# Optimization experiments

Hardware: AMD Instinct MI355X
Metric: run time of the kernel (lower is better)

## Reference

```python
import jax, jax.numpy as jnp
import numpy as np

N, E, IN, HID, H, L, CLS = 10000, 160000, 512, 128, 8, 4, 2
ALPHA = 0.1  # residual weight
BN_EPS = 1e-5
NEG_SLOPE = 0.2  # PyG GATConv leaky_relu default


def setup_inputs() -> dict:
    key = jax.random.key(0)
    ks = jax.random.split(key, 16)
    s = 0.05
    return {
        "x": jax.random.normal(ks[0], (N, IN), jnp.float32),
        "edge_index": jax.random.randint(ks[1], (2, E), 0, N, jnp.int64),
        "Wp": jax.random.normal(ks[2], (IN, HID), jnp.float32) * s,
        "bp": jax.random.normal(ks[3], (HID,), jnp.float32) * s,
        # stacked per-layer GATConv params (shared src/dst weight as in PyG)
        "Wl": jax.random.normal(ks[4], (L, HID, H * HID), jnp.float32) * s,
        "att_src": jax.random.normal(ks[5], (L, H, HID), jnp.float32) * s,
        "att_dst": jax.random.normal(ks[6], (L, H, HID), jnp.float32) * s,
        "bl": jax.random.normal(ks[7], (L, HID), jnp.float32) * s,
        # BatchNorm (eval mode: running_mean=0, running_var=1)
        "gamma": 1.0 + jax.random.normal(ks[8], (L, HID), jnp.float32) * s,
        "beta": jax.random.normal(ks[9], (L, HID), jnp.float32) * s,
        # classifier
        "W1": jax.random.normal(ks[10], (HID, HID // 2), jnp.float32) * s,
        "b1": jax.random.normal(ks[11], (HID // 2,), jnp.float32) * s,
        "W2": jax.random.normal(ks[12], (HID // 2, CLS), jnp.float32) * s,
        "b2": jax.random.normal(ks[13], (CLS,), jnp.float32) * s,
    }


def gat_layer(h, src, dst, W, a_src, a_dst, bias):
    # h: [N, HID]; W: [HID, H*HID]
    xl = (h @ W).reshape(N, H, HID)                 # [N, H, C]
    alpha_s = jnp.sum(xl * a_src[None], axis=-1)     # [N, H]
    alpha_d = jnp.sum(xl * a_dst[None], axis=-1)     # [N, H]
    e = jax.nn.leaky_relu(alpha_s[src] + alpha_d[dst], NEG_SLOPE)  # [E', H]
    # segment softmax over incoming edges of each dst node
    emax = jax.ops.segment_max(e, dst, num_segments=N)
    ee = jnp.exp(e - emax[dst])
    denom = jax.ops.segment_sum(ee, dst, num_segments=N)
    att = ee / (denom[dst] + 1e-16)                  # [E', H]
    msg = xl[src] * att[:, :, None]                  # [E', H, C]
    out = jax.ops.segment_sum(msg, dst, num_segments=N)  # [N, H, C]
    return out.mean(axis=1) + bias                   # concat=False -> mean over heads


def reference(x, edge_index, Wp, bp, Wl, att_src, att_dst, bl, gamma, beta, W1, b1, W2, b2):
    # add self-loops (PyG GATConv default add_self_loops=True)
    loop = jnp.arange(N, dtype=edge_index.dtype)
    src = jnp.concatenate([edge_index[0], loop])
    dst = jnp.concatenate([edge_index[1], loop])

    h = jax.nn.elu(x @ Wp + bp)
    bn_inv = 1.0 / jnp.sqrt(1.0 + BN_EPS)
    for i in range(L):
        prev = h
        g = gat_layer(h, src, dst, Wl[i], att_src[i], att_dst[i], bl[i])
        g = gamma[i] * (g * bn_inv) + beta[i]        # BN eval (mean 0, var 1)
        h = jax.nn.elu((1.0 - ALPHA) * g + ALPHA * prev)
        # dropout is identity in eval mode
    hid = jax.nn.elu(h @ W1 + b1)
    return hid @ W2 + b2                             # [N, CLS]
```

## Files before the change

kernel.cpp:

```cpp
#include <hip/hip_runtime.h>
#include <cstdint>
#include <cstddef>

#define N_NODES 10000
#define N_EDGES 160000
#define DIM_IN  512
#define HIDDIM  128
#define NHEAD   8
#define NLAYER  4

typedef unsigned int  uint32;
typedef unsigned short ushort16;

static __device__ __forceinline__ float eluf(float v)  { return v > 0.f ? v : expm1f(v); }
static __device__ __forceinline__ float lrelu(float v) { return v >= 0.f ? v : 0.2f * v; }
static __device__ __forceinline__ ushort16 f2bf(float f) {
    uint32 u = __float_as_uint(f);
    u += 0x7fffu + ((u >> 16) & 1u);
    return (ushort16)(u >> 16);
}

#define BN_INV 0.9999950000374997f

__global__ void k_deg(const int* __restrict__ ei, int* __restrict__ deg) {
    int t = blockIdx.x * 256 + threadIdx.x;
    if (t < N_EDGES) atomicAdd(&deg[ei[N_EDGES + t]], 1);
}

__global__ __launch_bounds__(1024) void k_scan(const int* __restrict__ deg,
                                               int* __restrict__ rowptr,
                                               int* __restrict__ cursor) {
    __shared__ int sd[1024];
    __shared__ int carry;
    int tid = threadIdx.x;
    if (tid == 0) { carry = 0; rowptr[0] = 0; }
    __syncthreads();
    for (int base = 0; base < N_NODES; base += 1024) {
        int i = base + tid;
        int v = (i < N_NODES) ? (deg[i] + 1) : 0;
        sd[tid] = v;
        __syncthreads();
        for (int ofs = 1; ofs < 1024; ofs <<= 1) {
            int t = (tid >= ofs) ? sd[tid - ofs] : 0;
            __syncthreads();
            sd[tid] += t;
            __syncthreads();
        }
        int inc = sd[tid] + carry;
        if (i < N_NODES) { rowptr[i + 1] = inc; cursor[i] = inc - v; }
        __syncthreads();
        if (tid == 1023) carry = inc;
        __syncthreads();
    }
}

__global__ void k_scatter(const int* __restrict__ ei, int* __restrict__ cursor,
                          int* __restrict__ csr) {
    int t = blockIdx.x * 256 + threadIdx.x;
    if (t < N_EDGES) {
        int s = ei[t];
        int d = ei[N_EDGES + t];
        int p = atomicAdd(&cursor[d], 1);
        csr[p] = s;
    } else if (t < N_EDGES + N_NODES) {
        int n = t - N_EDGES;
        int p = atomicAdd(&cursor[n], 1);
        csr[p] = n;
    }
}

template <int ACT, int OUTBF>
__global__ __launch_bounds__(256) void k_gemm(const float* __restrict__ A,
                                              const float* __restrict__ B,
                                              const float* __restrict__ bias,
                                              void* __restrict__ Cv,
                                              int M, int Nn, int K) {
    __shared__ float As[16][64];
    __shared__ float Bs[16][64];
    const int tx = threadIdx.x & 15;
    const int ty = threadIdx.x >> 4;
    const int row0 = blockIdx.y * 64, col0 = blockIdx.x * 64;
    const int la_m = threadIdx.x >> 2;
    const int la_k = (threadIdx.x & 3) * 4;
    const int lb_k = threadIdx.x >> 4;
    const int lb_n = (threadIdx.x & 15) * 4;
    float acc[4][4] = {};
    for (int k0 = 0; k0 < K; k0 += 16) {
        float4 av = make_float4(0.f, 0.f, 0.f, 0.f);
        int ar = row0 + la_m;
        if (ar < M) av = *(const float4*)(A + (size_t)ar * K + k0 + la_k);
        As[la_k + 0][la_m] = av.x;
        As[la_k + 1][la_m] = av.y;
        As[la_k + 2][la_m] = av.z;
        As[la_k + 3][la_m] = av.w;
        *(float4*)&Bs[lb_k][lb_n] = *(const float4*)(B + (size_t)(k0 + lb_k) * Nn + col0 + lb_n);
        __syncthreads();
#pragma unroll
        for (int k = 0; k < 16; k++) {
            float a[4], b[4];
#pragma unroll
            for (int i = 0; i < 4; i++) a[i] = As[k][ty * 4 + i];
#pragma unroll
            for (int j = 0; j < 4; j++) b[j] = Bs[k][tx * 4 + j];
#pragma unroll
            for (int i = 0; i < 4; i++)
#pragma unroll
                for (int j = 0; j < 4; j++) acc[i][j] += a[i] * b[j];
        }
        __syncthreads();
    }
#pragma unroll
    for (int i = 0; i < 4; i++) {
        int r = row0 + ty * 4 + i;
        if (r < M) {
            if (OUTBF) {
                ushort4 o;
                o.x = f2bf(acc[i][0]);
                o.y = f2bf(acc[i][1]);
                o.z = f2bf(acc[i][2]);
                o.w = f2bf(acc[i][3]);
                *(ushort4*)((ushort16*)Cv + (size_t)r * Nn + col0 + tx * 4) = o;
            } else {
                float4 o;
                float* op = (float*)&o;
#pragma unroll
                for (int j = 0; j < 4; j++) {
                    float v = acc[i][j];
                    if (ACT) {
                        v += bias[col0 + tx * 4 + j];
                        v = eluf(v);
                    }
                    op[j] = v;
                }
                *(float4*)((float*)Cv + (size_t)r * Nn + col0 + tx * 4) = o;
            }
        }
    }
}

__global__ __launch_bounds__(256) void k_alphas(const ushort16* __restrict__ xl,
                                                const float* __restrict__ atts,
                                                const float* __restrict__ attd,
                                                float* __restrict__ as_,
                                                float* __restrict__ ad_) {
    int lane = threadIdx.x & 63;
    int n = blockIdx.x * 4 + (threadIdx.x >> 6);
    if (n >= N_NODES) return;
    int g = lane >> 4;
    int c8 = 8 * (lane & 15);
    const uint4* xp = (const uint4*)(xl + (size_t)n * 1024);
    float ss[2], sd[2];
#pragma unroll
    for (int j = 0; j < 2; j++) {
        int head = 4 * j + g;
        uint4 u = xp[j * 64 + lane];
        const float4* ap = (const float4*)(atts + head * 128 + c8);
        const float4* bp = (const float4*)(attd + head * 128 + c8);
        float4 a0 = ap[0], a1 = ap[1];
        float4 b0 = bp[0], b1 = bp[1];
        float x0 = __uint_as_float(u.x << 16), x1 = __uint_as_float(u.x & 0xffff0000u);
        float x2 = __uint_as_float(u.y << 16), x3 = __uint_as_float(u.y & 0xffff0000u);
        float x4 = __uint_as_float(u.z << 16), x5 = __uint_as_float(u.z & 0xffff0000u);
        float x6 = __uint_as_float(u.w << 16), x7 = __uint_as_float(u.w & 0xffff0000u);
        ss[j] = x0 * a0.x + x1 * a0.y + x2 * a0.z + x3 * a0.w +
                x4 * a1.x + x5 * a1.y + x6 * a1.z + x7 * a1.w;
        sd[j] = x0 * b0.x + x1 * b0.y + x2 * b0.z + x3 * b0.w +
                x4 * b1.x + x5 * b1.y + x6 * b1.z + x7 * b1.w;
    }
#pragma unroll
    for (int m = 1; m < 16; m <<= 1) {
#pragma unroll
        for (int j = 0; j < 2; j++) {
            ss[j] += __shfl_xor(ss[j], m);
            sd[j] += __shfl_xor(sd[j], m);
        }
    }
    if ((lane & 15) == 0) {
        as_[n * 8 + g]     = ss[0];
        as_[n * 8 + 4 + g] = ss[1];
        ad_[n * 8 + g]     = sd[0];
        ad_[n * 8 + 4 + g] = sd[1];
    }
}

__global__ __launch_bounds__(256) void k_aggregate(const int* __restrict__ rowptr,
                                                   const int* __restrict__ csr,
                                                   const float* __restrict__ as_,
                                                   const float* __restrict__ ad_,
                                                   const ushort16* __restrict__ xl,
                                                   const float* __restrict__ hprev,
                                                   const float* __restrict__ bl,
                                                   const float* __restrict__ gam,
                                                   const float* __restrict__ bet,
                                                   float* __restrict__ hnext) {
    int lane = threadIdx.x & 63;
    int n = blockIdx.x * 4 + (threadIdx.x >> 6);
    if (n >= N_NODES) return;
    int h8 = lane & 7;
    int g = lane >> 4;
    float adh = ad_[n * 8 + h8];
    int start = rowptr[n], end = rowptr[n + 1];

    float acc0[8] = {}, acc1[8] = {};
    float denom = 0.f;
    int s = (start < end) ? csr[start] : 0;
    for (int e = start; e < end; ++e) {
        int sn = (e + 1 < end) ? csr[e + 1] : 0;
        float t = lrelu(as_[s * 8 + h8] + adh);
        float ee = __expf(t);
        denom += ee;
        float e0 = __shfl(ee, g);
        float e1 = __shfl(ee, 4 + g);
        const uint4* xp = (const uint4*)(xl + (size_t)s * 1024);
        uint4 u0 = xp[lane];
        uint4 u1 = xp[64 + lane];
        acc0[0] += e0 * __uint_as_float(u0.x << 16);
        acc0[1] += e0 * __uint_as_float(u0.x & 0xffff0000u);
        acc0[2] += e0 * __uint_as_float(u0.y << 16);
        acc0[3] += e0 * __uint_as_float(u0.y & 0xffff0000u);
        acc0[4] += e0 * __uint_as_float(u0.z << 16);
        acc0[5] += e0 * __uint_as_float(u0.z & 0xffff0000u);
        acc0[6] += e0 * __uint_as_float(u0.w << 16);
        acc0[7] += e0 * __uint_as_float(u0.w & 0xffff0000u);
        acc1[0] += e1 * __uint_as_float(u1.x << 16);
        acc1[1] += e1 * __uint_as_float(u1.x & 0xffff0000u);
        acc1[2] += e1 * __uint_as_float(u1.y << 16);
        acc1[3] += e1 * __uint_as_float(u1.y & 0xffff0000u);
        acc1[4] += e1 * __uint_as_float(u1.z << 16);
        acc1[5] += e1 * __uint_as_float(u1.z & 0xffff0000u);
        acc1[6] += e1 * __uint_as_float(u1.w << 16);
        acc1[7] += e1 * __uint_as_float(u1.w & 0xffff0000u);
        s = sn;
    }

    float d0 = __shfl(denom, g);
    float d1 = __shfl(denom, 4 + g);
    float r0 = 1.f / (d0 + 1e-16f);
    float r1 = 1.f / (d1 + 1e-16f);
    float sum[8];
#pragma unroll
    for (int i = 0; i < 8; i++) sum[i] = acc0[i] * r0 + acc1[i] * r1;
#pragma unroll
    for (int i = 0; i < 8; i++) {
        sum[i] += __shfl_xor(sum[i], 16);
        sum[i] += __shfl_xor(sum[i], 32);
    }

    if (lane < 16) {
        int c = 8 * lane;
        float o[8];
#pragma unroll
        for (int t = 0; t < 8; t++) {
            float m = sum[t] * 0.125f + bl[c + t];
            float gg = gam[c + t] * (m * BN_INV) + bet[c + t];
            float z = 0.9f * gg + 0.1f * hprev[(size_t)n * 128 + c + t];
            o[t] = eluf(z);
        }
        *(float4*)(hnext + (size_t)n * 128 + c)     = make_float4(o[0], o[1], o[2], o[3]);
        *(float4*)(hnext + (size_t)n * 128 + c + 4) = make_float4(o[4], o[5], o[6], o[7]);
    }
}

__global__ __launch_bounds__(256) void k_classifier(const float* __restrict__ h,
                                                    const float* __restrict__ W1,
                                                    const float* __restrict__ b1,
                                                    const float* __restrict__ W2,
                                                    const float* __restrict__ b2,
                                                    float* __restrict__ out) {
    __shared__ float sW1[128 * 64];
    __shared__ float sW2[128];
    __shared__ float sb1[64];
    __shared__ float sb2[2];
    for (int i = threadIdx.x; i < 2048; i += 256)
        *(float4*)&sW1[i * 4] = *(const float4*)(W1 + i * 4);
    if (threadIdx.x < 64) sb1[threadIdx.x] = b1[threadIdx.x];
    if (threadIdx.x < 128) sW2[threadIdx.x] = W2[threadIdx.x];
    if (threadIdx.x < 2) sb2[threadIdx.x] = b2[threadIdx.x];
    __syncthreads();
    int lane = threadIdx.x & 63;
    int n = blockIdx.x * 4 + (threadIdx.x >> 6);
    if (n >= N_NODES) return;
    float h0 = h[(size_t)n * 128 + lane];
    float h1 = h[(size_t)n * 128 + 64 + lane];
    float acc = sb1[lane];
#pragma unroll
    for (int c = 0; c < 64; c++) acc += __shfl(h0, c) * sW1[c * 64 + lane];
#pragma unroll
    for (int c = 0; c < 64; c++) acc += __shfl(h1, c) * sW1[(64 + c) * 64 + lane];
    acc = eluf(acc);
    float p0 = acc * sW2[lane * 2 + 0];
    float p1 = acc * sW2[lane * 2 + 1];
#pragma unroll
    for (int m = 1; m < 64; m <<= 1) {
        p0 += __shfl_xor(p0, m);
        p1 += __shfl_xor(p1, m);
    }
    if (lane == 0) {
        out[(size_t)n * 2 + 0] = p0 + sb2[0];
        out[(size_t)n * 2 + 1] = p1 + sb2[1];
    }
}

extern "C" void kernel_launch(void* const* d_in, const int* in_sizes, int n_in,
                              void* d_out, int out_size, void* d_ws, size_t ws_size,
                              hipStream_t stream) {
    const float* x       = (const float*)d_in[0];
    const int* ei        = (const int*)d_in[1];
    const float* Wp      = (const float*)d_in[2];
    const float* bp      = (const float*)d_in[3];
    const float* Wl      = (const float*)d_in[4];
    const float* atts    = (const float*)d_in[5];
    const float* attd    = (const float*)d_in[6];
    const float* bl      = (const float*)d_in[7];
    const float* gam     = (const float*)d_in[8];
    const float* bet     = (const float*)d_in[9];
    const float* W1      = (const float*)d_in[10];
    const float* b1      = (const float*)d_in[11];
    const float* W2      = (const float*)d_in[12];
    const float* b2      = (const float*)d_in[13];
    float* out = (float*)d_out;

    char* w = (char*)d_ws;
    auto carve = [&](size_t bytes) -> void* {
        void* p = (void*)w;
        w += (bytes + 255) & ~(size_t)255;
        return p;
    };
    int* deg        = (int*)carve((size_t)N_NODES * 4);
    int* rowptr     = (int*)carve((size_t)(N_NODES + 1) * 4);
    int* cursor     = (int*)carve((size_t)N_NODES * 4);
    int* csr        = (int*)carve((size_t)(N_EDGES + N_NODES) * 4);
    float* as_      = (float*)carve((size_t)N_NODES * 8 * 4);
    float* ad_      = (float*)carve((size_t)N_NODES * 8 * 4);
    ushort16* xl    = (ushort16*)carve((size_t)N_NODES * 1024 * 2);
    float* hA       = (float*)carve((size_t)N_NODES * 128 * 4);
    float* hB       = (float*)carve((size_t)N_NODES * 128 * 4);

    hipMemsetAsync(deg, 0, (size_t)N_NODES * 4, stream);
    k_deg<<<(N_EDGES + 255) / 256, 256, 0, stream>>>(ei, deg);
    k_scan<<<1, 1024, 0, stream>>>(deg, rowptr, cursor);
    k_scatter<<<(N_EDGES + N_NODES + 255) / 256, 256, 0, stream>>>(ei, cursor, csr);

    k_gemm<1, 0><<<dim3(2, 157), 256, 0, stream>>>(x, Wp, bp, hA, N_NODES, 128, 512);

    float* hc = hA;
    float* hn = hB;
    for (int l = 0; l < NLAYER; l++) {
        k_gemm<0, 1><<<dim3(16, 157), 256, 0, stream>>>(hc, Wl + (size_t)l * 128 * 1024, nullptr,
                                                        xl, N_NODES, 1024, 128);
        k_alphas<<<2500, 256, 0, stream>>>(xl, atts + l * 1024, attd + l * 1024, as_, ad_);
        k_aggregate<<<2500, 256, 0, stream>>>(rowptr, csr, as_, ad_, xl, hc, bl + l * 128,
                                              gam + l * 128, bet + l * 128, hn);
        float* tmp = hc; hc = hn; hn = tmp;
    }
    k_classifier<<<2500, 256, 0, stream>>>(hc, W1, b1, W2, b2, out);
}
```

Measured before the change: 585.1 us.

## Use bf16 MFMA GEMM with swizzled LDS and unroll aggregation loop by two

Replaces the scalar FP32 tiled GEMM with a bf16 MFMA 16x16x32 kernel. It stages A and B tiles in LDS as bf16 with an XOR swizzle and a K-tile of 128, so the projection and per-layer GATConv matmuls run on matrix cores. The aggregate loop is also unrolled two edges at a time so gathers for two neighbours are in flight together. Rounding inputs to bf16 lowers GEMM precision, including the first projection, which was FP32 before.

```diff
diff --git a/kernel.cpp b/kernel.cpp
--- a/kernel.cpp
+++ b/kernel.cpp
@@ -9,8 +9,10 @@
 #define NHEAD   8
 #define NLAYER  4
 
-typedef unsigned int  uint32;
+typedef unsigned int   uint32;
 typedef unsigned short ushort16;
+typedef __attribute__((ext_vector_type(8))) short bf16x8;
+typedef __attribute__((ext_vector_type(4))) float f32x4;
 
 static __device__ __forceinline__ float eluf(float v)  { return v > 0.f ? v : expm1f(v); }
 static __device__ __forceinline__ float lrelu(float v) { return v >= 0.f ? v : 0.2f * v; }
@@ -19,6 +21,8 @@
     u += 0x7fffu + ((u >> 16) & 1u);
     return (ushort16)(u >> 16);
 }
+static __device__ __forceinline__ float blo(uint32 u) { return __uint_as_float(u << 16); }
+static __device__ __forceinline__ float bhi(uint32 u) { return __uint_as_float(u & 0xffff0000u); }
 
 #define BN_INV 0.9999950000374997f
 
@@ -70,69 +74,79 @@
 }
 
 template <int ACT, int OUTBF>
-__global__ __launch_bounds__(256) void k_gemm(const float* __restrict__ A,
-                                              const float* __restrict__ B,
-                                              const float* __restrict__ bias,
-                                              void* __restrict__ Cv,
-                                              int M, int Nn, int K) {
-    __shared__ float As[16][64];
-    __shared__ float Bs[16][64];
-    const int tx = threadIdx.x & 15;
-    const int ty = threadIdx.x >> 4;
+__global__ __launch_bounds__(256) void k_gemm_mfma(const float* __restrict__ A,
+                                                   const float* __restrict__ B,
+                                                   const float* __restrict__ bias,
+                                                   void* __restrict__ Cv,
+                                                   int M, int Nn, int K) {
+    __shared__ unsigned short AsU[64 * 128];
+    __shared__ unsigned short BsU[64 * 128];
+    char* AsB = (char*)AsU;
+    char* BsB = (char*)BsU;
+    const int tid = threadIdx.x;
+    const int lane = tid & 63;
+    const int wv = tid >> 6;
     const int row0 = blockIdx.y * 64, col0 = blockIdx.x * 64;
-    const int la_m = threadIdx.x >> 2;
-    const int la_k = (threadIdx.x & 3) * 4;
-    const int lb_k = threadIdx.x >> 4;
-    const int lb_n = (threadIdx.x & 15) * 4;
-    float acc[4][4] = {};
-    for (int k0 = 0; k0 < K; k0 += 16) {
-        float4 av = make_float4(0.f, 0.f, 0.f, 0.f);
-        int ar = row0 + la_m;
-        if (ar < M) av = *(const float4*)(A + (size_t)ar * K + k0 + la_k);
-        As[la_k + 0][la_m] = av.x;
-        As[la_k + 1][la_m] = av.y;
-        As[la_k + 2][la_m] = av.z;
-        As[la_k + 3][la_m] = av.w;
-        *(float4*)&Bs[lb_k][lb_n] = *(const float4*)(B + (size_t)(k0 + lb_k) * Nn + col0 + lb_n);
-        __syncthreads();
-#pragma unroll
-        for (int k = 0; k < 16; k++) {
-            float a[4], b[4];
-#pragma unroll
-            for (int i = 0; i < 4; i++) a[i] = As[k][ty * 4 + i];
-#pragma unroll
-            for (int j = 0; j < 4; j++) b[j] = Bs[k][tx * 4 + j];
-#pragma unroll
-            for (int i = 0; i < 4; i++)
-#pragma unroll
-                for (int j = 0; j < 4; j++) acc[i][j] += a[i] * b[j];
-        }
-        __syncthreads();
-    }
-#pragma unroll
-    for (int i = 0; i < 4; i++) {
-        int r = row0 + ty * 4 + i;
-        if (r < M) {
-            if (OUTBF) {
-                ushort4 o;
-                o.x = f2bf(acc[i][0]);
-                o.y = f2bf(acc[i][1]);
-                o.z = f2bf(acc[i][2]);
-                o.w = f2bf(acc[i][3]);
-                *(ushort4*)((ushort16*)Cv + (size_t)r * Nn + col0 + tx * 4) = o;
-            } else {
-                float4 o;
-                float* op = (float*)&o;
-#pragma unroll
-                for (int j = 0; j < 4; j++) {
-                    float v = acc[i][j];
-                    if (ACT) {
-                        v += bias[col0 + tx * 4 + j];
-                        v = eluf(v);
-                    }
-                    op[j] = v;
-                }
-                *(float4*)((float*)Cv + (size_t)r * Nn + col0 + tx * 4) = o;
+    const int r = lane & 15, q = lane >> 4;
+
+    f32x4 acc[4];
+#pragma unroll
+    for (int i = 0; i < 4; i++) acc[i] = (f32x4){0.f, 0.f, 0.f, 0.f};
+
+    for (int k0 = 0; k0 < K; k0 += 128) {
+        __syncthreads();
+#pragma unroll
+        for (int it = 0; it < 8; it++) {
+            int gq = tid + it * 256;
+            int row = gq >> 5;
+            int k4 = (gq & 31) * 4;
+            int gr = row0 + row;
+            float4 v = make_float4(0.f, 0.f, 0.f, 0.f);
+            if (gr < M) v = *(const float4*)(A + (size_t)gr * K + k0 + k4);
+            ushort4 o;
+            o.x = f2bf(v.x); o.y = f2bf(v.y); o.z = f2bf(v.z); o.w = f2bf(v.w);
+            int byte = (row * 256 + k4 * 2) ^ ((row & 7) << 4);
+            *(ushort4*)(AsB + byte) = o;
+        }
+#pragma unroll
+        for (int it = 0; it < 8; it++) {
+            int gq = tid + it * 256;
+            int kk = gq >> 4;
+            int c4 = (gq & 15) * 4;
+            float4 v = *(const float4*)(B + (size_t)(k0 + kk) * Nn + col0 + c4);
+            float vv[4] = {v.x, v.y, v.z, v.w};
+#pragma unroll
+            for (int c = 0; c < 4; c++) {
+                int col = c4 + c;
+                int byte = (col * 256 + kk * 2) ^ ((col & 7) << 4);
+                *(unsigned short*)(BsB + byte) = f2bf(vv[c]);
+            }
+        }
+        __syncthreads();
+#pragma unroll
+        for (int ks = 0; ks < 4; ks++) {
+            int kb = (ks * 32 + q * 8) * 2;
+            int arow = wv * 16 + r;
+            bf16x8 af = *(bf16x8*)(AsB + ((arow * 256 + kb) ^ ((arow & 7) << 4)));
+#pragma unroll
+            for (int nb = 0; nb < 4; nb++) {
+                int col = nb * 16 + r;
+                bf16x8 bfr = *(bf16x8*)(BsB + ((col * 256 + kb) ^ ((col & 7) << 4)));
+                acc[nb] = __builtin_amdgcn_mfma_f32_16x16x32_bf16(af, bfr, acc[nb], 0, 0, 0);
+            }
+        }
+    }
+#pragma unroll
+    for (int nb = 0; nb < 4; nb++) {
+        int col = col0 + nb * 16 + r;
+#pragma unroll
+        for (int j = 0; j < 4; j++) {
+            int row = row0 + wv * 16 + q * 4 + j;
+            if (row < M) {
+                float v = acc[nb][j];
+                if (ACT) { v += bias[col]; v = eluf(v); }
+                if (OUTBF) ((unsigned short*)Cv)[(size_t)row * Nn + col] = f2bf(v);
+                else       ((float*)Cv)[(size_t)row * Nn + col] = v;
             }
         }
     }
@@ -158,10 +172,8 @@
         const float4* bp = (const float4*)(attd + head * 128 + c8);
         float4 a0 = ap[0], a1 = ap[1];
         float4 b0 = bp[0], b1 = bp[1];
-        float x0 = __uint_as_float(u.x << 16), x1 = __uint_as_float(u.x & 0xffff0000u);
-        float x2 = __uint_as_float(u.y << 16), x3 = __uint_as_float(u.y & 0xffff0000u);
-        float x4 = __uint_as_float(u.z << 16), x5 = __uint_as_float(u.z & 0xffff0000u);
-        float x6 = __uint_as_float(u.w << 16), x7 = __uint_as_float(u.w & 0xffff0000u);
+        float x0 = blo(u.x), x1 = bhi(u.x), x2 = blo(u.y), x3 = bhi(u.y);
+        float x4 = blo(u.z), x5 = bhi(u.z), x6 = blo(u.w), x7 = bhi(u.w);
         ss[j] = x0 * a0.x + x1 * a0.y + x2 * a0.z + x3 * a0.w +
                 x4 * a1.x + x5 * a1.y + x6 * a1.z + x7 * a1.w;
         sd[j] = x0 * b0.x + x1 * b0.y + x2 * b0.z + x3 * b0.w +
@@ -203,34 +215,56 @@
 
     float acc0[8] = {}, acc1[8] = {};
     float denom = 0.f;
-    int s = (start < end) ? csr[start] : 0;
-    for (int e = start; e < end; ++e) {
-        int sn = (e + 1 < end) ? csr[e + 1] : 0;
-        float t = lrelu(as_[s * 8 + h8] + adh);
-        float ee = __expf(t);
-        denom += ee;
-        float e0 = __shfl(ee, g);
-        float e1 = __shfl(ee, 4 + g);
-        const uint4* xp = (const uint4*)(xl + (size_t)s * 1024);
-        uint4 u0 = xp[lane];
-        uint4 u1 = xp[64 + lane];
-        acc0[0] += e0 * __uint_as_float(u0.x << 16);
-        acc0[1] += e0 * __uint_as_float(u0.x & 0xffff0000u);
-        acc0[2] += e0 * __uint_as_float(u0.y << 16);
-        acc0[3] += e0 * __uint_as_float(u0.y & 0xffff0000u);
-        acc0[4] += e0 * __uint_as_float(u0.z << 16);
-        acc0[5] += e0 * __uint_as_float(u0.z & 0xffff0000u);
-        acc0[6] += e0 * __uint_as_float(u0.w << 16);
-        acc0[7] += e0 * __uint_as_float(u0.w & 0xffff0000u);
-        acc1[0] += e1 * __uint_as_float(u1.x << 16);
-        acc1[1] += e1 * __uint_as_float(u1.x & 0xffff0000u);
-        acc1[2] += e1 * __uint_as_float(u1.y << 16);
-        acc1[3] += e1 * __uint_as_float(u1.y & 0xffff0000u);
-        acc1[4] += e1 * __uint_as_float(u1.z << 16);
-        acc1[5] += e1 * __uint_as_float(u1.z & 0xffff0000u);
-        acc1[6] += e1 * __uint_as_float(u1.w << 16);
-        acc1[7] += e1 * __uint_as_float(u1.w & 0xffff0000u);
-        s = sn;
+    int e = start;
+    int s0 = csr[e];
+    int s1 = (e + 1 < end) ? csr[e + 1] : 0;
+    for (; e + 1 < end; e += 2) {
+        int s2 = (e + 2 < end) ? csr[e + 2] : 0;
+        int s3 = (e + 3 < end) ? csr[e + 3] : 0;
+        float as0 = as_[s0 * 8 + h8];
+        float as1 = as_[s1 * 8 + h8];
+        const uint4* xp0 = (const uint4*)(xl + (size_t)s0 * 1024);
+        const uint4* xp1 = (const uint4*)(xl + (size_t)s1 * 1024);
+        uint4 u0a = xp0[lane], u1a = xp0[64 + lane];
+        uint4 u0b = xp1[lane], u1b = xp1[64 + lane];
+        float ee0 = __expf(lrelu(as0 + adh));
+        float ee1 = __expf(lrelu(as1 + adh));
+        denom += ee0 + ee1;
+        float e0a = __shfl(ee0, g), e1a = __shfl(ee0, 4 + g);
+        float e0b = __shfl(ee1, g), e1b = __shfl(ee1, 4 + g);
+        acc0[0] += e0a * blo(u0a.x); acc0[1] += e0a * bhi(u0a.x);
+        acc0[2] += e0a * blo(u0a.y); acc0[3] += e0a * bhi(u0a.y);
+        acc0[4] += e0a * blo(u0a.z); acc0[5] += e0a * bhi(u0a.z);
+        acc0[6] += e0a * blo(u0a.w); acc0[7] += e0a * bhi(u0a.w);
+        acc1[0] += e1a * blo(u1a.x); acc1[1] += e1a * bhi(u1a.x);
+        acc1[2] += e1a * blo(u1a.y); acc1[3] += e1a * bhi(u1a.y);
+        acc1[4] += e1a * blo(u1a.z); acc1[5] += e1a * bhi(u1a.z);
+        acc1[6] += e1a * blo(u1a.w); acc1[7] += e1a * bhi(u1a.w);
+        acc0[0] += e0b * blo(u0b.x); acc0[1] += e0b * bhi(u0b.x);
+        acc0[2] += e0b * blo(u0b.y); acc0[3] += e0b * bhi(u0b.y);
+        acc0[4] += e0b * blo(u0b.z); acc0[5] += e0b * bhi(u0b.z);
+        acc0[6] += e0b * blo(u0b.w); acc0[7] += e0b * bhi(u0b.w);
+        acc1[0] += e1b * blo(u1b.x); acc1[1] += e1b * bhi(u1b.x);
+        acc1[2] += e1b * blo(u1b.y); acc1[3] += e1b * bhi(u1b.y);
+        acc1[4] += e1b * blo(u1b.z); acc1[5] += e1b * bhi(u1b.z);
+        acc1[6] += e1b * blo(u1b.w); acc1[7] += e1b * bhi(u1b.w);
+        s0 = s2; s1 = s3;
+    }
+    if (e < end) {
+        float as0 = as_[s0 * 8 + h8];
+        const uint4* xp0 = (const uint4*)(xl + (size_t)s0 * 1024);
+        uint4 u0a = xp0[lane], u1a = xp0[64 + lane];
+        float ee0 = __expf(lrelu(as0 + adh));
+        denom += ee0;
+        float e0a = __shfl(ee0, g), e1a = __shfl(ee0, 4 + g);
+        acc0[0] += e0a * blo(u0a.x); acc0[1] += e0a * bhi(u0a.x);
+        acc0[2] += e0a * blo(u0a.y); acc0[3] += e0a * bhi(u0a.y);
+        acc0[4] += e0a * blo(u0a.z); acc0[5] += e0a * bhi(u0a.z);
+        acc0[6] += e0a * blo(u0a.w); acc0[7] += e0a * bhi(u0a.w);
+        acc1[0] += e1a * blo(u1a.x); acc1[1] += e1a * bhi(u1a.x);
+        acc1[2] += e1a * blo(u1a.y); acc1[3] += e1a * bhi(u1a.y);
+        acc1[4] += e1a * blo(u1a.z); acc1[5] += e1a * bhi(u1a.z);
+        acc1[6] += e1a * blo(u1a.w); acc1[7] += e1a * bhi(u1a.w);
     }
 
     float d0 = __shfl(denom, g);
@@ -341,13 +375,13 @@
     k_scan<<<1, 1024, 0, stream>>>(deg, rowptr, cursor);
     k_scatter<<<(N_EDGES + N_NODES + 255) / 256, 256, 0, stream>>>(ei, cursor, csr);
 
-    k_gemm<1, 0><<<dim3(2, 157), 256, 0, stream>>>(x, Wp, bp, hA, N_NODES, 128, 512);
+    k_gemm_mfma<1, 0><<<dim3(2, 157), 256, 0, stream>>>(x, Wp, bp, hA, N_NODES, 128, 512);
 
     float* hc = hA;
     float* hn = hB;
     for (int l = 0; l < NLAYER; l++) {
-        k_gemm<0, 1><<<dim3(16, 157), 256, 0, stream>>>(hc, Wl + (size_t)l * 128 * 1024, nullptr,
-                                                        xl, N_NODES, 1024, 128);
+        k_gemm_mfma<0, 1><<<dim3(16, 157), 256, 0, stream>>>(hc, Wl + (size_t)l * 128 * 1024,
+                                                             nullptr, xl, N_NODES, 1024, 128);
         k_alphas<<<2500, 256, 0, stream>>>(xl, atts + l * 1024, attd + l * 1024, as_, ad_);
         k_aggregate<<<2500, 256, 0, stream>>>(rowptr, csr, as_, ad_, xl, hc, bl + l * 128,
                                               gam + l * 128, bet + l * 128, hn);
```

Result: faster. 504.3 us (-13.8%).
